# Optimization experiments

Measured on AMD Instinct MI355X. Metric: run time of the kernel, lower is better.

## Reference

```python
import jax, jax.numpy as jnp
import numpy as np

N, M, D = 4096, 4096, 8

def laplace_tensor_markov(x, grid, lengthscale):
    # product over dims of exp(-|x_i - y_j|/ls) == exp(-sum_d |x_id - y_jd|/ls_d)
    # x: [n,d], grid: [m,d] -> [n,m]
    diff = jnp.abs(x[:, None, :] - grid[None, :, :]) / lengthscale  # [n,m,d]
    return jnp.exp(-jnp.sum(diff, axis=-1))

def setup_inputs() -> dict:
    key = jax.random.key(0)
    k1, k2, k3 = jax.random.split(key, 3)
    x = jax.random.normal(k1, (N, D), dtype=jnp.float32)
    sparse_grid = jax.random.uniform(k2, (M, D), dtype=jnp.float32)
    # inverse Cholesky factor is lower-triangular; emulate its structured sparsity
    L = jax.random.normal(k3, (M, M), dtype=jnp.float32) * 0.02
    chol_inv = jnp.tril(L) + jnp.eye(M, dtype=jnp.float32)
    lengthscale = jnp.ones((D,), dtype=jnp.float32)
    return {"x": x, "sparse_grid": sparse_grid, "chol_inv": chol_inv, "lengthscale": lengthscale}

def reference(x, sparse_grid, chol_inv, lengthscale):
    k_star = laplace_tensor_markov(x, sparse_grid, lengthscale)  # [n,m]
    phi = k_star @ chol_inv                                      # [n,m]
    return phi
```

## Files before the change

kernel.cpp:

```cpp
#include <hip/hip_runtime.h>
#include <cstdint>
#include <cstddef>

typedef unsigned short u16;
typedef __bf16 bf16x8 __attribute__((ext_vector_type(8)));
typedef float floatx4 __attribute__((ext_vector_type(4)));

#define NPTS 4096
#define MGRD 4096
#define DDIM 8

static __device__ __forceinline__ u16 f2bf(float f) {
    uint32_t u = __float_as_uint(f);
    u += 0x7fffu + ((u >> 16) & 1u);
    return (u16)(u >> 16);
}

__global__ __launch_bounds__(256) void prep_kernel(
    const float* __restrict__ x, const float* __restrict__ g,
    const float* __restrict__ ls, const float* __restrict__ B,
    u16* __restrict__ A, u16* __restrict__ Bt)
{
    __shared__ float tile[64][65];
    const int bid = blockIdx.x;
    const int tid = threadIdx.x;

    if (bid < 512) {
        const int kb = bid & 1;
        const int n0 = (bid >> 1) * 16;
        const int k0 = kb * 2048 + tid * 8;

        float il[DDIM];
#pragma unroll
        for (int d = 0; d < DDIM; ++d) il[d] = 1.0f / ls[d];

        float4 g0[8], g1[8];
#pragma unroll
        for (int r = 0; r < 8; ++r) {
            g0[r] = *reinterpret_cast<const float4*>(g + (size_t)(k0 + r) * DDIM);
            g1[r] = *reinterpret_cast<const float4*>(g + (size_t)(k0 + r) * DDIM + 4);
        }

        for (int nn = 0; nn < 16; ++nn) {
            const int n = n0 + nn;
            const float4 x0 = *reinterpret_cast<const float4*>(x + (size_t)n * DDIM);
            const float4 x1 = *reinterpret_cast<const float4*>(x + (size_t)n * DDIM + 4);
            alignas(16) u16 res[8];
#pragma unroll
            for (int r = 0; r < 8; ++r) {
                float s = fabsf(x0.x - g0[r].x) * il[0] + fabsf(x0.y - g0[r].y) * il[1]
                        + fabsf(x0.z - g0[r].z) * il[2] + fabsf(x0.w - g0[r].w) * il[3]
                        + fabsf(x1.x - g1[r].x) * il[4] + fabsf(x1.y - g1[r].y) * il[5]
                        + fabsf(x1.z - g1[r].z) * il[6] + fabsf(x1.w - g1[r].w) * il[7];
                res[r] = f2bf(__expf(-s));
            }
            *reinterpret_cast<uint4*>(A + (size_t)n * MGRD + k0) =
                *reinterpret_cast<const uint4*>(res);
        }
    } else {
        const int id = bid - 512;
        const int bx = id & 63;
        const int by = id >> 6;
        if (by < (bx & ~1)) return;
        const int k0 = by * 64;
        const int m0 = bx * 64;

#pragma unroll
        for (int r = 0; r < 4; ++r) {
            int c   = r * 256 + tid;
            int row = c >> 4;
            int col = (c & 15) * 4;
            const float4 v = *reinterpret_cast<const float4*>(&B[(size_t)(k0 + row) * MGRD + m0 + col]);
            tile[row][col + 0] = v.x; tile[row][col + 1] = v.y;
            tile[row][col + 2] = v.z; tile[row][col + 3] = v.w;
        }
        __syncthreads();

#pragma unroll
        for (int r = 0; r < 2; ++r) {
            int c  = r * 256 + tid;
            int mr = c >> 3;
            int kc = (c & 7) * 8;
            alignas(16) u16 tmp[8];
#pragma unroll
            for (int j = 0; j < 8; ++j)
                tmp[j] = f2bf(tile[kc + j][mr]);
            *reinterpret_cast<uint4*>(&Bt[(size_t)(m0 + mr) * MGRD + k0 + kc]) =
                *reinterpret_cast<const uint4*>(tmp);
        }
    }
}


#define FENCE() asm volatile("" ::: "memory")
static __device__ __forceinline__ void bar() {
    FENCE(); __builtin_amdgcn_s_barrier(); FENCE();
}

__global__ __launch_bounds__(512, 2) void gemm_kh_kernel(
    const u16* __restrict__ A,
    const u16* __restrict__ Bt,
    float* __restrict__ C)
{
    __shared__ u16 lds[3 * 24576] __attribute__((aligned(16)));

    const int tid  = threadIdx.x;
    const int lane = tid & 63;
    const int w    = tid >> 6;
    const int kg   = w >> 2;
    const int wq   = w & 3;
    const int nq   = wq >> 1;
    const int mq   = wq & 1;
    const int lrow = lane & 15;
    const int lhi  = lane >> 4;
    const int r7   = lrow & 7;

    const int id  = blockIdx.x;
    const int bm  = id >> 4;
    const int bn  = id & 15;
    const int bn0 = bn << 8;
    const int bm0 = bm << 7;
    const int L   = 64 - 2 * bm;

    const int arow = tid >> 3;
    const int aswz = ((tid ^ arow) & 7) * 8;
    int aoff[4], boff[2];
#pragma unroll
    for (int r = 0; r < 4; ++r)
        aoff[r] = (bn0 + r * 64 + arow) * 4096 + aswz;
#pragma unroll
    for (int r = 0; r < 2; ++r)
        boff[r] = (bm0 + r * 64 + arow) * 4096 + aswz;

    const int ldst = w * 512;
    const int cswz = ((kg * 4 + lhi) ^ r7) * 8;
    const int rowA = (nq * 128 + lrow) * 64 + cswz;
    const int rowB = (mq * 64  + lrow) * 64 + cswz;

#define STG_A(QA, R, K) __builtin_amdgcn_global_load_lds(                        \
    (const __attribute__((address_space(1))) void*)(A + (size_t)aoff[R] + (K)),  \
    (__attribute__((address_space(3))) void*)((QA) + (R) * 4096 + ldst), 16, 0, 0)
#define STG_B(QB, R, K) __builtin_amdgcn_global_load_lds(                        \
    (const __attribute__((address_space(1))) void*)(Bt + (size_t)boff[R] + (K)), \
    (__attribute__((address_space(3))) void*)((QB) + (R) * 4096 + ldst), 16, 0, 0)

    bf16x8 af[4], bfv[4];

#define RDA(PA, IB) do {                                                         \
    af[0] = *reinterpret_cast<const bf16x8*>((PA) + rowA + ((IB) + 0) * 1024);   \
    af[1] = *reinterpret_cast<const bf16x8*>((PA) + rowA + ((IB) + 1) * 1024);   \
    af[2] = *reinterpret_cast<const bf16x8*>((PA) + rowA + ((IB) + 2) * 1024);   \
    af[3] = *reinterpret_cast<const bf16x8*>((PA) + rowA + ((IB) + 3) * 1024);   \
} while (0)
#define RDB(PB) do {                                                             \
    bfv[0] = *reinterpret_cast<const bf16x8*>((PB) + rowB + 0 * 1024);           \
    bfv[1] = *reinterpret_cast<const bf16x8*>((PB) + rowB + 1 * 1024);           \
    bfv[2] = *reinterpret_cast<const bf16x8*>((PB) + rowB + 2 * 1024);           \
    bfv[3] = *reinterpret_cast<const bf16x8*>((PB) + rowB + 3 * 1024);           \
} while (0)

    floatx4 acc[8][4];
#pragma unroll
    for (int i = 0; i < 8; ++i)
#pragma unroll
        for (int j = 0; j < 4; ++j)
            acc[i][j] = (floatx4)0.0f;

#define MF(a, b, c) __builtin_amdgcn_mfma_f32_16x16x32_bf16(a, b, c, 0, 0, 0)
#define MFMA16(IB) do {                                                          \
    __builtin_amdgcn_s_setprio(1);                                               \
    acc[(IB)+0][0] = MF(af[0], bfv[0], acc[(IB)+0][0]);                          \
    acc[(IB)+0][1] = MF(af[0], bfv[1], acc[(IB)+0][1]);                          \
    acc[(IB)+0][2] = MF(af[0], bfv[2], acc[(IB)+0][2]);                          \
    acc[(IB)+0][3] = MF(af[0], bfv[3], acc[(IB)+0][3]);                          \
    acc[(IB)+1][0] = MF(af[1], bfv[0], acc[(IB)+1][0]);                          \
    acc[(IB)+1][1] = MF(af[1], bfv[1], acc[(IB)+1][1]);                          \
    acc[(IB)+1][2] = MF(af[1], bfv[2], acc[(IB)+1][2]);                          \
    acc[(IB)+1][3] = MF(af[1], bfv[3], acc[(IB)+1][3]);                          \
    acc[(IB)+2][0] = MF(af[2], bfv[0], acc[(IB)+2][0]);                          \
    acc[(IB)+2][1] = MF(af[2], bfv[1], acc[(IB)+2][1]);                          \
    acc[(IB)+2][2] = MF(af[2], bfv[2], acc[(IB)+2][2]);                          \
    acc[(IB)+2][3] = MF(af[2], bfv[3], acc[(IB)+2][3]);                          \
    acc[(IB)+3][0] = MF(af[3], bfv[0], acc[(IB)+3][0]);                          \
    acc[(IB)+3][1] = MF(af[3], bfv[1], acc[(IB)+3][1]);                          \
    acc[(IB)+3][2] = MF(af[3], bfv[2], acc[(IB)+3][2]);                          \
    acc[(IB)+3][3] = MF(af[3], bfv[3], acc[(IB)+3][3]);                          \
    __builtin_amdgcn_s_setprio(0);                                               \
} while (0)

    int kT = 4096 - 64;
    {
        u16* qA0 = lds;                 u16* qB0 = lds + 16384;
        u16* qA1 = lds + 24576;         u16* qB1 = lds + 24576 + 16384;
        STG_A(qA0, 0, kT); STG_A(qA0, 1, kT); STG_A(qA0, 2, kT); STG_A(qA0, 3, kT);
        STG_B(qB0, 0, kT); STG_B(qB0, 1, kT);
        STG_A(qA1, 0, kT - 64); STG_A(qA1, 1, kT - 64);
        STG_A(qA1, 2, kT - 64); STG_A(qA1, 3, kT - 64);
        STG_B(qB1, 0, kT - 64); STG_B(qB1, 1, kT - 64);
    }
    asm volatile("s_waitcnt vmcnt(6)" ::: "memory");
    bar();

    int p = 0;
    for (int T = 0; T < L - 2; ++T) {
        u16* pA = lds + p * 24576;      u16* pB = pA + 16384;
        int p2 = p + 2; if (p2 >= 3) p2 -= 3;
        u16* qA = lds + p2 * 24576;     u16* qB = qA + 16384;
        const int kst = kT - 128;

        RDA(pA, 0); RDB(pB);
        STG_A(qA, 0, kst); STG_A(qA, 1, kst); STG_B(qB, 0, kst);
        bar();
        MFMA16(0);
        bar();
        RDA(pA, 4);
        STG_A(qA, 2, kst); STG_A(qA, 3, kst); STG_B(qB, 1, kst);
        bar();
        MFMA16(4);
        asm volatile("s_waitcnt vmcnt(6)" ::: "memory");
        bar();

        kT -= 64; ++p; if (p == 3) p = 0;
    }

    {
        u16* pA = lds + p * 24576;      u16* pB = pA + 16384;
        RDA(pA, 0); RDB(pB);
        bar();
        MFMA16(0);
        bar();
        RDA(pA, 4);
        bar();
        MFMA16(4);
        asm volatile("s_waitcnt vmcnt(0)" ::: "memory");
        bar();
        kT -= 64; ++p; if (p == 3) p = 0;
    }
    {
        u16* pA = lds + p * 24576;      u16* pB = pA + 16384;
        RDA(pA, 0); RDB(pB);
        bar();
        MFMA16(0);
        bar();
        RDA(pA, 4);
        bar();
        MFMA16(4);
    }

    __syncthreads();
    float* scr = reinterpret_cast<float*>(lds);
    if (kg == 1) {
#pragma unroll
        for (int i = 0; i < 8; ++i)
#pragma unroll
            for (int j = 0; j < 4; ++j)
                *reinterpret_cast<floatx4*>(
                    scr + (size_t)wq * 8192 + (i * 4 + j) * 256 + lane * 4) = acc[i][j];
    }
    __syncthreads();
    if (kg == 0) {
#pragma unroll
        for (int i = 0; i < 8; ++i)
#pragma unroll
            for (int j = 0; j < 4; ++j)
                acc[i][j] += *reinterpret_cast<const floatx4*>(
                    scr + (size_t)wq * 8192 + (i * 4 + j) * 256 + lane * 4);

#pragma unroll
        for (int i = 0; i < 8; ++i) {
            int rown = bn0 + nq * 128 + i * 16 + lhi * 4;
#pragma unroll
            for (int j = 0; j < 4; ++j) {
                int colm = bm0 + mq * 64 + j * 16 + lrow;
                float* cp = C + (size_t)rown * 4096 + colm;
#pragma unroll
                for (int rr = 0; rr < 4; ++rr)
                    cp[(size_t)rr * 4096] = acc[i][j][rr];
            }
        }
    }
}

extern "C" void kernel_launch(void* const* d_in, const int* in_sizes, int n_in,
                              void* d_out, int out_size, void* d_ws, size_t ws_size,
                              hipStream_t stream)
{
    const float* x    = (const float*)d_in[0];
    const float* grid = (const float*)d_in[1];
    const float* ci   = (const float*)d_in[2];
    const float* ls   = (const float*)d_in[3];
    float* out = (float*)d_out;

    u16* wsA  = (u16*)d_ws;
    u16* wsBt = (u16*)d_ws + (size_t)MGRD * MGRD;

    prep_kernel<<<dim3(512 + 64 * 64), 256, 0, stream>>>(x, grid, ls, ci, wsA, wsBt);
    gemm_kh_kernel<<<dim3(512), 512, 0, stream>>>(wsA, wsBt, out);
}
```

Measured before the change: 189.7 us.

## Collapse per-tile GEMM loop to single barrier with all fragments loaded upfront

The main loop changes from two half-steps, each with its own LDS fragment reads and three barriers, to one step. That step issues all global-to-LDS prefetches, reads all eight A fragments and four B fragments, runs 32 MFMAs, then hits one barrier. The aim is to cut barrier stalls per K-tile and let the MFMA chain run without interruption. The cost is more live VGPRs for fragments, which could pressure the 2-waves-per-SIMD occupancy target, and less interleaving of LDS reads with MFMAs.

Result: faster. 185.1 us (-2.4%).

```diff
diff --git a/kernel.cpp b/kernel.cpp
--- a/kernel.cpp
+++ b/kernel.cpp
@@ -97,7 +97,7 @@
     FENCE(); __builtin_amdgcn_s_barrier(); FENCE();
 }
 
-__global__ __launch_bounds__(512, 2) void gemm_kh_kernel(
+__global__ __launch_bounds__(512, 2) void gemm_sb_kernel(
     const u16* __restrict__ A,
     const u16* __restrict__ Bt,
     float* __restrict__ C)
@@ -144,19 +144,21 @@
     (const __attribute__((address_space(1))) void*)(Bt + (size_t)boff[R] + (K)), \
     (__attribute__((address_space(3))) void*)((QB) + (R) * 4096 + ldst), 16, 0, 0)
 
-    bf16x8 af[4], bfv[4];
-
-#define RDA(PA, IB) do {                                                         \
-    af[0] = *reinterpret_cast<const bf16x8*>((PA) + rowA + ((IB) + 0) * 1024);   \
-    af[1] = *reinterpret_cast<const bf16x8*>((PA) + rowA + ((IB) + 1) * 1024);   \
-    af[2] = *reinterpret_cast<const bf16x8*>((PA) + rowA + ((IB) + 2) * 1024);   \
-    af[3] = *reinterpret_cast<const bf16x8*>((PA) + rowA + ((IB) + 3) * 1024);   \
-} while (0)
-#define RDB(PB) do {                                                             \
+    bf16x8 af[8], bfv[4];
+
+#define RDALL(PA, PB) do {                                                       \
+    af[0]  = *reinterpret_cast<const bf16x8*>((PA) + rowA + 0 * 1024);           \
     bfv[0] = *reinterpret_cast<const bf16x8*>((PB) + rowB + 0 * 1024);           \
     bfv[1] = *reinterpret_cast<const bf16x8*>((PB) + rowB + 1 * 1024);           \
     bfv[2] = *reinterpret_cast<const bf16x8*>((PB) + rowB + 2 * 1024);           \
     bfv[3] = *reinterpret_cast<const bf16x8*>((PB) + rowB + 3 * 1024);           \
+    af[1]  = *reinterpret_cast<const bf16x8*>((PA) + rowA + 1 * 1024);           \
+    af[2]  = *reinterpret_cast<const bf16x8*>((PA) + rowA + 2 * 1024);           \
+    af[3]  = *reinterpret_cast<const bf16x8*>((PA) + rowA + 3 * 1024);           \
+    af[4]  = *reinterpret_cast<const bf16x8*>((PA) + rowA + 4 * 1024);           \
+    af[5]  = *reinterpret_cast<const bf16x8*>((PA) + rowA + 5 * 1024);           \
+    af[6]  = *reinterpret_cast<const bf16x8*>((PA) + rowA + 6 * 1024);           \
+    af[7]  = *reinterpret_cast<const bf16x8*>((PA) + rowA + 7 * 1024);           \
 } while (0)
 
     floatx4 acc[8][4];
@@ -167,24 +169,13 @@
             acc[i][j] = (floatx4)0.0f;
 
 #define MF(a, b, c) __builtin_amdgcn_mfma_f32_16x16x32_bf16(a, b, c, 0, 0, 0)
-#define MFMA16(IB) do {                                                          \
+#define MFMA32() do {                                                            \
     __builtin_amdgcn_s_setprio(1);                                               \
-    acc[(IB)+0][0] = MF(af[0], bfv[0], acc[(IB)+0][0]);                          \
-    acc[(IB)+0][1] = MF(af[0], bfv[1], acc[(IB)+0][1]);                          \
-    acc[(IB)+0][2] = MF(af[0], bfv[2], acc[(IB)+0][2]);                          \
-    acc[(IB)+0][3] = MF(af[0], bfv[3], acc[(IB)+0][3]);                          \
-    acc[(IB)+1][0] = MF(af[1], bfv[0], acc[(IB)+1][0]);                          \
-    acc[(IB)+1][1] = MF(af[1], bfv[1], acc[(IB)+1][1]);                          \
-    acc[(IB)+1][2] = MF(af[1], bfv[2], acc[(IB)+1][2]);                          \
-    acc[(IB)+1][3] = MF(af[1], bfv[3], acc[(IB)+1][3]);                          \
-    acc[(IB)+2][0] = MF(af[2], bfv[0], acc[(IB)+2][0]);                          \
-    acc[(IB)+2][1] = MF(af[2], bfv[1], acc[(IB)+2][1]);                          \
-    acc[(IB)+2][2] = MF(af[2], bfv[2], acc[(IB)+2][2]);                          \
-    acc[(IB)+2][3] = MF(af[2], bfv[3], acc[(IB)+2][3]);                          \
-    acc[(IB)+3][0] = MF(af[3], bfv[0], acc[(IB)+3][0]);                          \
-    acc[(IB)+3][1] = MF(af[3], bfv[1], acc[(IB)+3][1]);                          \
-    acc[(IB)+3][2] = MF(af[3], bfv[2], acc[(IB)+3][2]);                          \
-    acc[(IB)+3][3] = MF(af[3], bfv[3], acc[(IB)+3][3]);                          \
+    _Pragma("unroll")                                                            \
+    for (int i_ = 0; i_ < 8; ++i_)                                               \
+        _Pragma("unroll")                                                        \
+        for (int j_ = 0; j_ < 4; ++j_)                                           \
+            acc[i_][j_] = MF(af[i_], bfv[j_], acc[i_][j_]);                      \
     __builtin_amdgcn_s_setprio(0);                                               \
 } while (0)
 
@@ -208,15 +199,10 @@
         u16* qA = lds + p2 * 24576;     u16* qB = qA + 16384;
         const int kst = kT - 128;
 
-        RDA(pA, 0); RDB(pB);
-        STG_A(qA, 0, kst); STG_A(qA, 1, kst); STG_B(qB, 0, kst);
-        bar();
-        MFMA16(0);
-        bar();
-        RDA(pA, 4);
-        STG_A(qA, 2, kst); STG_A(qA, 3, kst); STG_B(qB, 1, kst);
-        bar();
-        MFMA16(4);
+        STG_A(qA, 0, kst); STG_A(qA, 1, kst); STG_A(qA, 2, kst); STG_A(qA, 3, kst);
+        STG_B(qB, 0, kst); STG_B(qB, 1, kst);
+        RDALL(pA, pB);
+        MFMA32();
         asm volatile("s_waitcnt vmcnt(6)" ::: "memory");
         bar();
 
@@ -225,26 +211,16 @@
 
     {
         u16* pA = lds + p * 24576;      u16* pB = pA + 16384;
-        RDA(pA, 0); RDB(pB);
-        bar();
-        MFMA16(0);
-        bar();
-        RDA(pA, 4);
-        bar();
-        MFMA16(4);
+        RDALL(pA, pB);
+        MFMA32();
         asm volatile("s_waitcnt vmcnt(0)" ::: "memory");
         bar();
-        kT -= 64; ++p; if (p == 3) p = 0;
+        ++p; if (p == 3) p = 0;
     }
     {
         u16* pA = lds + p * 24576;      u16* pB = pA + 16384;
-        RDA(pA, 0); RDB(pB);
-        bar();
-        MFMA16(0);
-        bar();
-        RDA(pA, 4);
-        bar();
-        MFMA16(4);
+        RDALL(pA, pB);
+        MFMA32();
     }
 
     __syncthreads();
@@ -295,5 +271,5 @@
     u16* wsBt = (u16*)d_ws + (size_t)MGRD * MGRD;
 
     prep_kernel<<<dim3(512 + 64 * 64), 256, 0, stream>>>(x, grid, ls, ci, wsA, wsBt);
-    gemm_kh_kernel<<<dim3(512), 512, 0, stream>>>(wsA, wsBt, out);
-}
+    gemm_sb_kernel<<<dim3(512), 512, 0, stream>>>(wsA, wsBt, out);
+}
```
